# Optimization experiments

Hardware: AMD Instinct MI355X
Metric: run time of the kernel (lower is better)

Reference implementation:

```python
import jax, jax.numpy as jnp
import numpy as np

B, C, HID, H, W = 8, 256, 256, 128, 128


def setup_inputs() -> dict:
    key = jax.random.key(0)
    ks = jax.random.split(key, 8)
    x = jax.random.normal(ks[0], (B, C, H, W), dtype=jnp.float32)
    prior = jax.random.normal(ks[1], (B, 1, H, W), dtype=jnp.float32)
    # xavier-uniform-style 1x1 conv weights: limit = sqrt(6/(fan_in+fan_out))
    lim_i = float(np.sqrt(6.0 / (C + HID)))
    lim_o = float(np.sqrt(6.0 / (HID + C)))
    Wi = jax.random.uniform(ks[2], (HID, C), minval=-lim_i, maxval=lim_i, dtype=jnp.float32)
    bi = jnp.zeros((HID,), dtype=jnp.float32)
    Wo = jax.random.uniform(ks[3], (C, HID), minval=-lim_o, maxval=lim_o, dtype=jnp.float32)
    bo = jnp.zeros((C,), dtype=jnp.float32)
    A_param = 0.1 * jax.random.normal(ks[4], (HID,), dtype=jnp.float32)
    B_param = 0.1 * jax.random.normal(ks[5], (HID,), dtype=jnp.float32)
    alpha = jnp.asarray(0.1, dtype=jnp.float32)
    gamma = jnp.asarray(0.1, dtype=jnp.float32)
    return {"x": x, "prior": prior, "Wi": Wi, "bi": bi, "A_param": A_param,
            "B_param": B_param, "alpha": alpha, "gamma": gamma, "Wo": Wo, "bo": bo}


def _lin_scan(u, a):
    """Linear recurrence h_t = a*h_{t-1} + u_t over leading axis.
    u: [T, B, Ch, X]; a: [Ch]."""
    a_b = a[None, :, None]  # broadcast over [B, Ch, X]
    def step(h, ut):
        h = a_b * h + ut
        return h, h
    _, hs = jax.lax.scan(step, jnp.zeros_like(u[0]), u)
    return hs  # [T, B, Ch, X]


def reference(x, prior, Wi, bi, A_param, B_param, alpha, gamma, Wo, bo):
    # prior is [B,1,H,W] at matching resolution -> only clamp applies
    p = jnp.clip(prior, -1.0, 1.0)
    F_mod = x + alpha * p  # broadcast over channel dim == expand
    # 1x1 conv input projection
    xp = jnp.einsum('bchw,oc->bohw', F_mod, Wi) + bi[None, :, None, None]
    A = jnp.tanh(A_param)
    u = B_param[None, :, None, None] * xp  # B*x term precomputed
    # horizontal recurrence (over width)
    uh = jnp.moveaxis(u, 3, 0)                       # [W,B,Ch,H]
    h_h = jnp.moveaxis(_lin_scan(uh, A), 0, 3)       # [B,Ch,H,W]
    # vertical recurrence (over height)
    uv = jnp.moveaxis(u, 2, 0)                       # [H,B,Ch,W]
    h_v = jnp.moveaxis(_lin_scan(uv, A), 0, 2)       # [B,Ch,H,W]
    h_fused = h_h + h_v
    out = jnp.einsum('bchw,oc->bohw', h_fused, Wo) + bo[None, :, None, None]
    return F_mod + gamma * out
```

## Files before the change

kernel.cpp:

```cpp
#include <hip/hip_runtime.h>
#include <hip/hip_bf16.h>
#include <math.h>


typedef unsigned int u32;
typedef unsigned short u16;
typedef __bf16 bf16x8 __attribute__((ext_vector_type(8)));
typedef float f32x4 __attribute__((ext_vector_type(4)));

__device__ __forceinline__ float bf2f(u16 r) { return __uint_as_float(((u32)r) << 16); }
__device__ __forceinline__ u16 f2bf(float f) {
    u32 x = __float_as_uint(f);
    return (u16)((x + 0x7FFFu + ((x >> 16) & 1u)) >> 16);
}
__device__ __forceinline__ float clip1(float v) { return fminf(1.f, fmaxf(-1.f, v)); }

__device__ __forceinline__ void gload16(const void* g, void* l) {
    __builtin_amdgcn_global_load_lds((__attribute__((address_space(1))) void*)g,
                                     (__attribute__((address_space(3))) void*)l, 16, 0, 0);
}

__global__ __launch_bounds__(256) void kw_conv(const float* __restrict__ Wi,
                                               const float* __restrict__ Wo,
                                               u16* __restrict__ Wib, u16* __restrict__ Wob) {
    int i = blockIdx.x * 256 + threadIdx.x;
    Wib[i] = f2bf(Wi[i]);
    Wob[i] = f2bf(Wo[i]);
}

#define SA_STRIDE 40
__global__ __launch_bounds__(512) void k01_gemm1(const float* __restrict__ x,
                                                 const float* __restrict__ prior,
                                                 const u16* __restrict__ Wib,
                                                 const float* __restrict__ bi,
                                                 const float* __restrict__ Bp,
                                                 const float* __restrict__ A_param,
                                                 const float* __restrict__ alpha_p,
                                                 u16* __restrict__ u, u16* __restrict__ hh) {
    __shared__ __align__(16) char smem[65536];
    u16* sA = (u16*)smem;
    u16* sB = (u16*)(smem + 20480);
    u16* ut = (u16*)smem;

    const int t = threadIdx.x;
    const int b = blockIdx.x >> 7, h = blockIdx.x & 127;
    const int wave = t >> 6, l = t & 63;
    const int wr = wave >> 2, wc = wave & 3;
    const int lr = l & 15, lg = l >> 4;

    const int cl = t & 31, w0 = (t >> 5) * 8;
    const float alpha = alpha_p[0];

    const float* prow = prior + (size_t)b * 16384 + h * 128 + w0;
    float fp[8];
    {
        float4 p0 = *(const float4*)prow;
        float4 p1 = *(const float4*)(prow + 4);
        fp[0] = alpha * clip1(p0.x); fp[1] = alpha * clip1(p0.y);
        fp[2] = alpha * clip1(p0.z); fp[3] = alpha * clip1(p0.w);
        fp[4] = alpha * clip1(p1.x); fp[5] = alpha * clip1(p1.y);
        fp[6] = alpha * clip1(p1.z); fp[7] = alpha * clip1(p1.w);
    }
    const float* xrow = x + ((size_t)b * 256 * 128 + h) * 128;

    f32x4 acc[4][4];
#pragma unroll
    for (int mi = 0; mi < 4; ++mi)
#pragma unroll
        for (int ni = 0; ni < 4; ++ni) acc[mi][ni] = (f32x4){0.f, 0.f, 0.f, 0.f};

    float4 xa, xb;
#define LOADX(ks)                                                        \
    do {                                                                 \
        const float* p_ = xrow + (size_t)((ks) * 32 + cl) * 16384 + w0;  \
        xa = *(const float4*)p_;                                         \
        xb = *(const float4*)(p_ + 4);                                   \
    } while (0)
#define CVTWR(buf)                                            \
    do {                                                      \
        u16* d_ = sA + (buf) * (128 * SA_STRIDE);             \
        d_[(w0 + 0) * SA_STRIDE + cl] = f2bf(xa.x + fp[0]);   \
        d_[(w0 + 1) * SA_STRIDE + cl] = f2bf(xa.y + fp[1]);   \
        d_[(w0 + 2) * SA_STRIDE + cl] = f2bf(xa.z + fp[2]);   \
        d_[(w0 + 3) * SA_STRIDE + cl] = f2bf(xa.w + fp[3]);   \
        d_[(w0 + 4) * SA_STRIDE + cl] = f2bf(xb.x + fp[4]);   \
        d_[(w0 + 5) * SA_STRIDE + cl] = f2bf(xb.y + fp[5]);   \
        d_[(w0 + 6) * SA_STRIDE + cl] = f2bf(xb.z + fp[6]);   \
        d_[(w0 + 7) * SA_STRIDE + cl] = f2bf(xb.w + fp[7]);   \
    } while (0)
#define STAGEB(buf, ks)                                                                     \
    do {                                                                                    \
        const int k0_ = (ks) * 32;                                                          \
        { const int s = t;                                                                  \
          gload16(&Wib[(size_t)(s >> 2) * 256 + k0_ + (s & 3) * 8],                         \
                  sB + (buf) * 8192 + s * 8); }                                             \
        { const int s = t + 512;                                                            \
          gload16(&Wib[(size_t)(s >> 2) * 256 + k0_ + (s & 3) * 8],                         \
                  sB + (buf) * 8192 + s * 8); }                                             \
    } while (0)

    LOADX(0);
    STAGEB(0, 0);
    CVTWR(0);
    __syncthreads();

    int cur = 0;
    for (int ks = 0; ks < 8; ++ks) {
        if (ks < 7) {
            LOADX(ks + 1);
            STAGEB(cur ^ 1, ks + 1);
        }
        bf16x8 af[4], bfv[4];
#pragma unroll
        for (int mi = 0; mi < 4; ++mi)
            af[mi] = *(const bf16x8*)&sA[cur * (128 * SA_STRIDE) +
                                         (wr * 64 + mi * 16 + lr) * SA_STRIDE + lg * 8];
#pragma unroll
        for (int ni = 0; ni < 4; ++ni)
            bfv[ni] = *(const bf16x8*)&sB[cur * 8192 + (wc * 64 + ni * 16 + lr) * 32 + lg * 8];
#pragma unroll
        for (int mi = 0; mi < 4; ++mi)
#pragma unroll
            for (int ni = 0; ni < 4; ++ni)
                acc[mi][ni] =
                    __builtin_amdgcn_mfma_f32_16x16x32_bf16(af[mi], bfv[ni], acc[mi][ni], 0, 0, 0);
        if (ks < 7) CVTWR(cur ^ 1);
        __syncthreads();
        cur ^= 1;
    }
#undef LOADX
#undef CVTWR
#undef STAGEB

    float bp4[4], bi4[4];
#pragma unroll
    for (int ni = 0; ni < 4; ++ni) {
        const int o = wc * 64 + ni * 16 + lr;
        bp4[ni] = Bp[o];
        bi4[ni] = bi[o];
    }
#pragma unroll
    for (int mi = 0; mi < 4; ++mi)
#pragma unroll
        for (int j = 0; j < 4; ++j) {
            const int w = wr * 64 + mi * 16 + lg * 4 + j;
#pragma unroll
            for (int ni = 0; ni < 4; ++ni) {
                const int o = wc * 64 + ni * 16 + lr;
                ut[w * 256 + o] = f2bf(bp4[ni] * (acc[mi][ni][j] + bi4[ni]));
            }
        }
    __syncthreads();

    const size_t gbase = ((size_t)b * 16384 + (size_t)h * 128) * 256;
    if (wave < 4) {
        const int o = t;
        const float A = tanhf(A_param[o]);
        float hacc = 0.f;
        for (int wb = 0; wb < 16; ++wb) {
            float v[8];
#pragma unroll
            for (int j = 0; j < 8; ++j) v[j] = bf2f(ut[(wb * 8 + j) * 256 + o]);
            u16 s8[8];
#pragma unroll
            for (int j = 0; j < 8; ++j) {
                hacc = fmaf(A, hacc, v[j]);
                s8[j] = f2bf(hacc);
            }
#pragma unroll
            for (int j = 0; j < 8; ++j) hh[gbase + (size_t)(wb * 8 + j) * 256 + o] = s8[j];
        }
    } else {
        const int t2 = t - 256;
        int4* ug = (int4*)(u + gbase);
        const int4* us = (const int4*)ut;
#pragma unroll
        for (int i = 0; i < 16; ++i) {
            const int chunk = t2 + 256 * i;
            ug[chunk] = us[chunk];
        }
    }
}

__global__ __launch_bounds__(256) void k2v(u16* __restrict__ u, const u16* __restrict__ hh,
                                           const float* __restrict__ A_param) {
    const int o = threadIdx.x;
    const int b = blockIdx.x >> 7, w = blockIdx.x & 127;
    const float A = tanhf(A_param[o]);
    size_t base = ((size_t)b * 16384 + w) * 256 + o;
    float hacc = 0.f;
    for (int hb = 0; hb < 16; ++hb) {
        float v[8], g[8];
#pragma unroll
        for (int j = 0; j < 8; ++j) {
            v[j] = bf2f(u[base + (size_t)j * 32768]);
            g[j] = bf2f(hh[base + (size_t)j * 32768]);
        }
        u16 w8[8];
#pragma unroll
        for (int j = 0; j < 8; ++j) {
            hacc = fmaf(A, hacc, v[j]);
            w8[j] = f2bf(hacc + g[j]);
        }
#pragma unroll
        for (int j = 0; j < 8; ++j) u[base + (size_t)j * 32768] = w8[j];
        base += (size_t)8 * 32768;
    }
}

__global__ __launch_bounds__(512) void k3_gemm2(const u16* __restrict__ hf,
                                                const u16* __restrict__ Wob,
                                                const float* __restrict__ x,
                                                const float* __restrict__ prior,
                                                const float* __restrict__ bo,
                                                const float* __restrict__ alpha_p,
                                                const float* __restrict__ gamma_p,
                                                float* __restrict__ out) {
    __shared__ __align__(16) u16 sA[2][256 * 32];
    __shared__ __align__(16) u16 sB[2][128 * 32];
    const int t = threadIdx.x;
    const int bx = blockIdx.x;
    const int b = bx >> 7, nt = bx & 127;
    const size_t Hbase = ((size_t)b * 16384 + (size_t)nt * 128) * 256;
    const int wave = t >> 6, l = t & 63;
    const int wr = wave >> 1, wc = wave & 1;
    const int lr = l & 15, lg = l >> 4;

    f32x4 acc[4][4];
#pragma unroll
    for (int mi = 0; mi < 4; ++mi)
#pragma unroll
        for (int ni = 0; ni < 4; ++ni) acc[mi][ni] = (f32x4){0.f, 0.f, 0.f, 0.f};

#define STAGE3(buf, ks)                                                                   \
    do {                                                                                  \
        const int k0_ = (ks) * 32;                                                        \
        { const int s = t;                                                                \
          gload16(&Wob[(size_t)(s >> 2) * 256 + k0_ + (s & 3) * 8], &sA[buf][s * 8]); }   \
        { const int s = t + 512;                                                          \
          gload16(&Wob[(size_t)(s >> 2) * 256 + k0_ + (s & 3) * 8], &sA[buf][s * 8]); }   \
        { const int s = t;                                                                \
          gload16(&hf[Hbase + (size_t)(s >> 2) * 256 + k0_ + (s & 3) * 8],                \
                  &sB[buf][s * 8]); }                                                     \
    } while (0)

    int cur = 0;
    STAGE3(0, 0);
    __syncthreads();
    for (int ks = 0; ks < 8; ++ks) {
        if (ks < 7) STAGE3(cur ^ 1, ks + 1);
        bf16x8 af[4], bfv[4];
#pragma unroll
        for (int mi = 0; mi < 4; ++mi)
            af[mi] = *(const bf16x8*)&sA[cur][(wr * 64 + mi * 16 + lr) * 32 + lg * 8];
#pragma unroll
        for (int ni = 0; ni < 4; ++ni)
            bfv[ni] = *(const bf16x8*)&sB[cur][(wc * 64 + ni * 16 + lr) * 32 + lg * 8];
#pragma unroll
        for (int mi = 0; mi < 4; ++mi)
#pragma unroll
            for (int ni = 0; ni < 4; ++ni)
                acc[mi][ni] =
                    __builtin_amdgcn_mfma_f32_16x16x32_bf16(af[mi], bfv[ni], acc[mi][ni], 0, 0, 0);
        __syncthreads();
        cur ^= 1;
    }
#undef STAGE3

    const float alpha = alpha_p[0], gamma = gamma_p[0];
    float pr4[4];
#pragma unroll
    for (int ni = 0; ni < 4; ++ni) {
        const int p_loc = wc * 64 + ni * 16 + lr;
        pr4[ni] = clip1(prior[(size_t)b * 16384 + (size_t)nt * 128 + p_loc]);
    }
#pragma unroll
    for (int mi = 0; mi < 4; ++mi)
#pragma unroll
        for (int j = 0; j < 4; ++j) {
            const int o = wr * 64 + mi * 16 + lg * 4 + j;
            const float bov = bo[o];
            const size_t obase = ((size_t)b * 256 + o) * 16384 + (size_t)nt * 128;
#pragma unroll
            for (int ni = 0; ni < 4; ++ni) {
                const int p_loc = wc * 64 + ni * 16 + lr;
                out[obase + p_loc] =
                    x[obase + p_loc] + alpha * pr4[ni] + gamma * (acc[mi][ni][j] + bov);
            }
        }
}

extern "C" void kernel_launch(void* const* d_in, const int* in_sizes, int n_in,
                              void* d_out, int out_size, void* d_ws, size_t ws_size,
                              hipStream_t stream) {
    const float* x = (const float*)d_in[0];
    const float* prior = (const float*)d_in[1];
    const float* Wi = (const float*)d_in[2];
    const float* bi = (const float*)d_in[3];
    const float* A_param = (const float*)d_in[4];
    const float* B_param = (const float*)d_in[5];
    const float* alpha = (const float*)d_in[6];
    const float* gamma = (const float*)d_in[7];
    const float* Wo = (const float*)d_in[8];
    const float* bo = (const float*)d_in[9];
    float* out = (float*)d_out;

    u16* u = (u16*)d_ws;
    u16* hh = (u16*)((char*)d_ws + 67108864ull);
    u16* Wib = (u16*)((char*)d_ws + 134217728ull);
    u16* Wob = (u16*)((char*)d_ws + 134348800ull);

    hipLaunchKernelGGL(kw_conv, dim3(256), dim3(256), 0, stream, Wi, Wo, Wib, Wob);
    hipLaunchKernelGGL(k01_gemm1, dim3(1024), dim3(512), 0, stream, x, prior, Wib, bi, B_param,
                       A_param, alpha, u, hh);
    hipLaunchKernelGGL(k2v, dim3(1024), dim3(256), 0, stream, u, hh, A_param);
    hipLaunchKernelGGL(k3_gemm2, dim3(1024), dim3(512), 0, stream, u, Wob, x, prior, bo, alpha,
                       gamma, out);
}
```

Before: 174.7 us.

## Move horizontal+vertical sum into GEMM2 B-load and vectorise vertical scan

The vertical scan kernel no longer reads the horizontal-scan buffer. It now only scans u in place, processing four channels per thread with 8-byte loads and stores. The second GEMM loads both scan results into registers, adds them, rounds to bf16 and writes the sum to shared memory, replacing the direct global-to-LDS load. This removes one full buffer read from the scan pass and widens its memory accesses. In exchange the GEMM does a register-staged load with extra ALU work and reads twice as much for its B operand.

```diff
diff --git a/kernel.cpp b/kernel.cpp
--- a/kernel.cpp
+++ b/kernel.cpp
@@ -182,33 +182,38 @@
     }
 }
 
-__global__ __launch_bounds__(256) void k2v(u16* __restrict__ u, const u16* __restrict__ hh,
+__global__ __launch_bounds__(256) void k2v(u16* __restrict__ u,
                                            const float* __restrict__ A_param) {
-    const int o = threadIdx.x;
-    const int b = blockIdx.x >> 7, w = blockIdx.x & 127;
-    const float A = tanhf(A_param[o]);
-    size_t base = ((size_t)b * 16384 + w) * 256 + o;
-    float hacc = 0.f;
+    const int t = threadIdx.x;
+    const int b = blockIdx.x >> 5, wg = blockIdx.x & 31;
+    const int w = wg * 4 + (t >> 6);
+    const int o4 = (t & 63) * 4;
+    const float A0 = tanhf(A_param[o4 + 0]);
+    const float A1 = tanhf(A_param[o4 + 1]);
+    const float A2 = tanhf(A_param[o4 + 2]);
+    const float A3 = tanhf(A_param[o4 + 3]);
+    float h0 = 0.f, h1 = 0.f, h2 = 0.f, h3 = 0.f;
+    size_t base = ((size_t)b * 16384 + w) * 256 + o4;
     for (int hb = 0; hb < 16; ++hb) {
-        float v[8], g[8];
+        ushort4 v[8];
+#pragma unroll
+        for (int j = 0; j < 8; ++j) v[j] = *(const ushort4*)&u[base + (size_t)j * 32768];
 #pragma unroll
         for (int j = 0; j < 8; ++j) {
-            v[j] = bf2f(u[base + (size_t)j * 32768]);
-            g[j] = bf2f(hh[base + (size_t)j * 32768]);
-        }
-        u16 w8[8];
-#pragma unroll
-        for (int j = 0; j < 8; ++j) {
-            hacc = fmaf(A, hacc, v[j]);
-            w8[j] = f2bf(hacc + g[j]);
-        }
-#pragma unroll
-        for (int j = 0; j < 8; ++j) u[base + (size_t)j * 32768] = w8[j];
+            h0 = fmaf(A0, h0, bf2f(v[j].x));
+            h1 = fmaf(A1, h1, bf2f(v[j].y));
+            h2 = fmaf(A2, h2, bf2f(v[j].z));
+            h3 = fmaf(A3, h3, bf2f(v[j].w));
+            ushort4 r;
+            r.x = f2bf(h0); r.y = f2bf(h1); r.z = f2bf(h2); r.w = f2bf(h3);
+            *(ushort4*)&u[base + (size_t)j * 32768] = r;
+        }
         base += (size_t)8 * 32768;
     }
 }
 
-__global__ __launch_bounds__(512) void k3_gemm2(const u16* __restrict__ hf,
+__global__ __launch_bounds__(512) void k3_gemm2(const u16* __restrict__ hv,
+                                                const u16* __restrict__ hh,
                                                 const u16* __restrict__ Wob,
                                                 const float* __restrict__ x,
                                                 const float* __restrict__ prior,
@@ -232,23 +237,46 @@
 #pragma unroll
         for (int ni = 0; ni < 4; ++ni) acc[mi][ni] = (f32x4){0.f, 0.f, 0.f, 0.f};
 
-#define STAGE3(buf, ks)                                                                   \
+#define STAGE3A(buf, ks)                                                                  \
     do {                                                                                  \
         const int k0_ = (ks) * 32;                                                        \
         { const int s = t;                                                                \
           gload16(&Wob[(size_t)(s >> 2) * 256 + k0_ + (s & 3) * 8], &sA[buf][s * 8]); }   \
         { const int s = t + 512;                                                          \
           gload16(&Wob[(size_t)(s >> 2) * 256 + k0_ + (s & 3) * 8], &sA[buf][s * 8]); }   \
-        { const int s = t;                                                                \
-          gload16(&hf[Hbase + (size_t)(s >> 2) * 256 + k0_ + (s & 3) * 8],                \
-                  &sB[buf][s * 8]); }                                                     \
-    } while (0)
+    } while (0)
+#define LOADB(ks)                                                                 \
+    do {                                                                          \
+        const size_t off_ = Hbase + (size_t)(t >> 2) * 256 + (ks) * 32 + (t & 3) * 8; \
+        va = *(const int4*)&hv[off_];                                             \
+        vb = *(const int4*)&hh[off_];                                             \
+    } while (0)
+#define ADDWR(buf)                                                                \
+    do {                                                                          \
+        u32 rw[4];                                                                \
+        const u32 aw[4] = {(u32)va.x, (u32)va.y, (u32)va.z, (u32)va.w};           \
+        const u32 bw[4] = {(u32)vb.x, (u32)vb.y, (u32)vb.z, (u32)vb.w};           \
+        _Pragma("unroll")                                                         \
+        for (int q = 0; q < 4; ++q) {                                             \
+            float lo = __uint_as_float(aw[q] << 16) + __uint_as_float(bw[q] << 16);           \
+            float hi = __uint_as_float(aw[q] & 0xFFFF0000u) + __uint_as_float(bw[q] & 0xFFFF0000u); \
+            rw[q] = (u32)f2bf(lo) | ((u32)f2bf(hi) << 16);                        \
+        }                                                                         \
+        *(int4*)&sB[buf][t * 8] = make_int4(rw[0], rw[1], rw[2], rw[3]);          \
+    } while (0)
+
+    int4 va, vb;
+    LOADB(0);
+    STAGE3A(0, 0);
+    ADDWR(0);
+    __syncthreads();
 
     int cur = 0;
-    STAGE3(0, 0);
-    __syncthreads();
     for (int ks = 0; ks < 8; ++ks) {
-        if (ks < 7) STAGE3(cur ^ 1, ks + 1);
+        if (ks < 7) {
+            LOADB(ks + 1);
+            STAGE3A(cur ^ 1, ks + 1);
+        }
         bf16x8 af[4], bfv[4];
 #pragma unroll
         for (int mi = 0; mi < 4; ++mi)
@@ -262,10 +290,13 @@
             for (int ni = 0; ni < 4; ++ni)
                 acc[mi][ni] =
                     __builtin_amdgcn_mfma_f32_16x16x32_bf16(af[mi], bfv[ni], acc[mi][ni], 0, 0, 0);
+        if (ks < 7) ADDWR(cur ^ 1);
         __syncthreads();
         cur ^= 1;
     }
-#undef STAGE3
+#undef STAGE3A
+#undef LOADB
+#undef ADDWR
 
     const float alpha = alpha_p[0], gamma = gamma_p[0];
     float pr4[4];
@@ -313,7 +344,7 @@
     hipLaunchKernelGGL(kw_conv, dim3(256), dim3(256), 0, stream, Wi, Wo, Wib, Wob);
     hipLaunchKernelGGL(k01_gemm1, dim3(1024), dim3(512), 0, stream, x, prior, Wib, bi, B_param,
                        A_param, alpha, u, hh);
-    hipLaunchKernelGGL(k2v, dim3(1024), dim3(256), 0, stream, u, hh, A_param);
-    hipLaunchKernelGGL(k3_gemm2, dim3(1024), dim3(512), 0, stream, u, Wob, x, prior, bo, alpha,
-                       gamma, out);
-}
+    hipLaunchKernelGGL(k2v, dim3(256), dim3(256), 0, stream, u, A_param);
+    hipLaunchKernelGGL(k3_gemm2, dim3(1024), dim3(512), 0, stream, u, hh, Wob, x, prior, bo,
+                       alpha, gamma, out);
+}
```

New measurement: 182.1 us. +4.2%, slower.
